# Kernel tuning notes

Measured on AMD Instinct MI355X. Metric: run time of the kernel, lower is better.

## Reference

```python
import jax, jax.numpy as jnp
import numpy as np

B, I, H, O = 65536, 128, 256, 256

def setup_inputs() -> dict:
    key = jax.random.key(0)
    ks = jax.random.split(key, 6)
    s_h = 1.0 / np.sqrt(I + H)
    return {
        "input": jax.random.normal(ks[0], (B, I), jnp.float32),
        "hidden": jax.random.normal(ks[1], (B, H), jnp.float32),
        "w_i2h": jax.random.uniform(ks[2], (4 * H, I + H), jnp.float32, -s_h, s_h),
        "b_i2h": jax.random.uniform(ks[3], (4 * H,), jnp.float32, -s_h, s_h),
        "w_i2o": jax.random.uniform(ks[4], (O, I + H), jnp.float32, -s_h, s_h),
        "b_i2o": jax.random.uniform(ks[5], (O,), jnp.float32, -s_h, s_h),
    }

def reference(input, hidden, w_i2h, b_i2h, w_i2o, b_i2o):
    # combined: [B, I+H]
    combined = jnp.concatenate([input, hidden], axis=1)
    gates = combined @ w_i2h.T + b_i2h            # [B, 4H]
    h, ig, fg, og = jnp.split(gates, 4, axis=1)   # each [B, H]
    ig = jax.nn.sigmoid(ig)
    fg = jax.nn.sigmoid(fg)
    og = jax.nn.sigmoid(og)
    h = jnp.tanh(h)
    new_hidden = og * jnp.tanh(fg * hidden + ig * h)
    output = jax.nn.log_softmax(combined @ w_i2o.T + b_i2o, axis=1)  # [B, O]
    return (output, new_hidden)
```

## Files before the change

kernel.cpp:

```cpp
#include <hip/hip_runtime.h>
#include <hip/hip_bf16.h>
#include <math.h>


typedef __attribute__((ext_vector_type(8))) short bf16x8;
typedef __attribute__((ext_vector_type(4))) float f32x4;

#define BM   64
#define NW1  393216
#define NW2  98304

__device__ __forceinline__ unsigned short f2bf(float f) {
    union { __hip_bfloat16 h; unsigned short u; } cv;
    cv.h = __float2bfloat16(f);
    return cv.u;
}
__device__ __forceinline__ float bf2f(unsigned short u) {
    union { __hip_bfloat16 h; unsigned short u; } cv;
    cv.u = u;
    return __bfloat162float(cv.h);
}
__device__ __forceinline__ float fsigmoid(float x) {
    return 1.0f / (1.0f + __expf(-x));
}
__device__ __forceinline__ float ftanh(float x) {
    return 1.0f - 2.0f / (__expf(2.0f * x) + 1.0f);
}
__device__ __forceinline__ bf16x8 pack8(float4 v0, float4 v1) {
    bf16x8 r;
    r[0] = (short)f2bf(v0.x); r[1] = (short)f2bf(v0.y);
    r[2] = (short)f2bf(v0.z); r[3] = (short)f2bf(v0.w);
    r[4] = (short)f2bf(v1.x); r[5] = (short)f2bf(v1.y);
    r[6] = (short)f2bf(v1.z); r[7] = (short)f2bf(v1.w);
    return r;
}

__global__ void conv_w(const float* __restrict__ w1, const float* __restrict__ w2,
                       unsigned short* __restrict__ wb) {
    int idx = blockIdx.x * 256 + threadIdx.x;
    const int n1 = NW1 / 4;
    float4 v;
    if (idx < n1) v = ((const float4*)w1)[idx];
    else          v = ((const float4*)w2)[idx - n1];
    ushort4 u;
    u.x = f2bf(v.x); u.y = f2bf(v.y); u.z = f2bf(v.z); u.w = f2bf(v.w);
    ((ushort4*)wb)[idx] = u;
}

__device__ __forceinline__ int lds_off(int row, int g) {
    return row * 768 + ((g ^ (row & 7)) << 4);
}

__launch_bounds__(256, 3)
__global__ void lstm_fused(const float* __restrict__ input,
                           const float* __restrict__ hidden,
                           const unsigned short* __restrict__ w1b,
                           const unsigned short* __restrict__ w2b,
                           const float* __restrict__ b1,
                           const float* __restrict__ b2,
                           float* __restrict__ out_ls,
                           float* __restrict__ out_nh)
{
    __shared__ __align__(16) unsigned short Ash[BM * 384];
    __shared__ float red_m[4][BM];
    __shared__ float red_s[4][BM];
    char* Ab = (char*)Ash;

    const int tid  = threadIdx.x;
    const int wave = tid >> 6;
    const int lane = tid & 63;
    const int l15  = lane & 15;
    const int quad = lane >> 4;
    const int rx   = l15 & 7;
    const size_t r0 = (size_t)blockIdx.x * BM;

    #pragma unroll
    for (int it = 0; it < 12; ++it) {
        int idx = it * 256 + tid;
        int row = idx / 48, g = idx % 48;
        const float* src = (g < 16) ? (input  + (r0 + row) * 128 + g * 8)
                                    : (hidden + (r0 + row) * 256 + (g - 16) * 8);
        float4 v0 = ((const float4*)src)[0];
        float4 v1 = ((const float4*)src)[1];
        *(bf16x8*)(Ab + lds_off(row, g)) = pack8(v0, v1);
    }
    __syncthreads();

    const int abase = l15 * 768;

    for (int phase = 0; phase < 5; ++phase) {
        f32x4 acc[4][4];
        #pragma unroll
        for (int i = 0; i < 4; ++i)
            #pragma unroll
            for (int j = 0; j < 4; ++j)
                acc[i][j] = (f32x4){0.f, 0.f, 0.f, 0.f};

        const unsigned short* bp[4];
        if (phase < 4) {
            int j0 = phase * 64 + wave * 16;
            #pragma unroll
            for (int q = 0; q < 4; ++q)
                bp[q] = w1b + (size_t)(q * 256 + j0 + l15) * 384 + quad * 8;
        } else {
            #pragma unroll
            for (int nt = 0; nt < 4; ++nt)
                bp[nt] = w2b + (size_t)(wave * 64 + nt * 16 + l15) * 384 + quad * 8;
        }

        auto loadB = [&](bf16x8* b, int kk) {
            #pragma unroll
            for (int nt = 0; nt < 4; ++nt)
                b[nt] = *(const bf16x8*)(bp[nt] + kk);
        };
        auto loadA = [&](bf16x8* a, int kk) {
            int go = (((kk >> 3) + quad) ^ rx) << 4;
            #pragma unroll
            for (int mt = 0; mt < 4; ++mt)
                a[mt] = *(const bf16x8*)(Ab + abase + mt * 12288 + go);
        };
        auto mfmas = [&](bf16x8* a, bf16x8* b) {
            #pragma unroll
            for (int mt = 0; mt < 4; ++mt)
                #pragma unroll
                for (int nt = 0; nt < 4; ++nt)
                    acc[mt][nt] = __builtin_amdgcn_mfma_f32_16x16x32_bf16(
                        a[mt], b[nt], acc[mt][nt], 0, 0, 0);
        };

        bf16x8 b0[4], b1f[4], a0[4], a1[4];
        loadB(b0, 0);
        #pragma unroll
        for (int kk = 0; kk < 384; kk += 64) {
            loadB(b1f, kk + 32);
            loadA(a0, kk);
            mfmas(a0, b0);
            if (kk + 64 < 384) loadB(b0, kk + 64);
            loadA(a1, kk + 32);
            mfmas(a1, b1f);
        }

        if (phase < 4) {
            int j = phase * 64 + wave * 16 + l15;
            float bq0 = b1[j], bq1 = b1[256 + j], bq2 = b1[512 + j], bq3 = b1[768 + j];
            int e = 128 + j, ge = e >> 3, oe = (e & 7) * 2;
            #pragma unroll
            for (int mt = 0; mt < 4; ++mt) {
                #pragma unroll
                for (int r = 0; r < 4; ++r) {
                    int rowl = mt * 16 + quad * 4 + r;
                    float hprev = bf2f(*(const unsigned short*)
                                       (Ab + lds_off(rowl, ge) + oe));
                    float hv  = ftanh(acc[mt][0][r] + bq0);
                    float igv = fsigmoid(acc[mt][1][r] + bq1);
                    float fgv = fsigmoid(acc[mt][2][r] + bq2);
                    float ogv = fsigmoid(acc[mt][3][r] + bq3);
                    out_nh[(r0 + rowl) * 256 + j] = ogv * ftanh(fgv * hprev + igv * hv);
                }
            }
        } else {
            float bo[4];
            #pragma unroll
            for (int nt = 0; nt < 4; ++nt) bo[nt] = b2[wave * 64 + nt * 16 + l15];
            #pragma unroll
            for (int mt = 0; mt < 4; ++mt)
                #pragma unroll
                for (int nt = 0; nt < 4; ++nt)
                    #pragma unroll
                    for (int r = 0; r < 4; ++r)
                        acc[mt][nt][r] += bo[nt];

            float pm[4][4], ps[4][4];
            #pragma unroll
            for (int mt = 0; mt < 4; ++mt)
                #pragma unroll
                for (int r = 0; r < 4; ++r) {
                    float m = acc[mt][0][r];
                    #pragma unroll
                    for (int nt = 1; nt < 4; ++nt) m = fmaxf(m, acc[mt][nt][r]);
                    pm[mt][r] = m;
                }
            #pragma unroll
            for (int mask = 1; mask < 16; mask <<= 1)
                #pragma unroll
                for (int mt = 0; mt < 4; ++mt)
                    #pragma unroll
                    for (int r = 0; r < 4; ++r)
                        pm[mt][r] = fmaxf(pm[mt][r], __shfl_xor(pm[mt][r], mask, 64));
            #pragma unroll
            for (int mt = 0; mt < 4; ++mt)
                #pragma unroll
                for (int r = 0; r < 4; ++r) {
                    float s = 0.f;
                    #pragma unroll
                    for (int nt = 0; nt < 4; ++nt)
                        s += __expf(acc[mt][nt][r] - pm[mt][r]);
                    ps[mt][r] = s;
                }
            #pragma unroll
            for (int mask = 1; mask < 16; mask <<= 1)
                #pragma unroll
                for (int mt = 0; mt < 4; ++mt)
                    #pragma unroll
                    for (int r = 0; r < 4; ++r)
                        ps[mt][r] += __shfl_xor(ps[mt][r], mask, 64);

            if (l15 == 0) {
                #pragma unroll
                for (int mt = 0; mt < 4; ++mt)
                    #pragma unroll
                    for (int r = 0; r < 4; ++r) {
                        int rowl = mt * 16 + quad * 4 + r;
                        red_m[wave][rowl] = pm[mt][r];
                        red_s[wave][rowl] = ps[mt][r];
                    }
            }
            __syncthreads();
            #pragma unroll
            for (int mt = 0; mt < 4; ++mt)
                #pragma unroll
                for (int r = 0; r < 4; ++r) {
                    int rowl = mt * 16 + quad * 4 + r;
                    float M = red_m[0][rowl];
                    #pragma unroll
                    for (int w = 1; w < 4; ++w) M = fmaxf(M, red_m[w][rowl]);
                    float S = 0.f;
                    #pragma unroll
                    for (int w = 0; w < 4; ++w)
                        S += red_s[w][rowl] * __expf(red_m[w][rowl] - M);
                    float lz = M + logf(S);
                    #pragma unroll
                    for (int nt = 0; nt < 4; ++nt)
                        out_ls[(r0 + rowl) * 256 + wave * 64 + nt * 16 + l15] =
                            acc[mt][nt][r] - lz;
                }
        }
    }
}

extern "C" void kernel_launch(void* const* d_in, const int* in_sizes, int n_in,
                              void* d_out, int out_size, void* d_ws, size_t ws_size,
                              hipStream_t stream) {
    const float* input  = (const float*)d_in[0];
    const float* hidden = (const float*)d_in[1];
    const float* w1     = (const float*)d_in[2];
    const float* b1     = (const float*)d_in[3];
    const float* w2     = (const float*)d_in[4];
    const float* b2     = (const float*)d_in[5];
    float* out = (float*)d_out;
    unsigned short* wb = (unsigned short*)d_ws;

    conv_w<<<dim3((NW1 + NW2) / 4 / 256), dim3(256), 0, stream>>>(w1, w2, wb);
    lstm_fused<<<dim3(65536 / BM), dim3(256), 0, stream>>>(
        input, hidden, wb, wb + NW1, b1, b2,
        out, out + (size_t)65536 * 256);
}
```

Before: 377.5 us.

## Split each block's rows across two wave groups with 512 threads

New measurement: 442.1 us. 1.17x slower.

```diff
diff --git a/kernel.cpp b/kernel.cpp
--- a/kernel.cpp
+++ b/kernel.cpp
@@ -51,7 +51,7 @@
     return row * 768 + ((g ^ (row & 7)) << 4);
 }
 
-__launch_bounds__(256, 3)
+__launch_bounds__(512, 4)
 __global__ void lstm_fused(const float* __restrict__ input,
                            const float* __restrict__ hidden,
                            const unsigned short* __restrict__ w1b,
@@ -68,6 +68,8 @@
 
     const int tid  = threadIdx.x;
     const int wave = tid >> 6;
+    const int wj   = wave & 3;
+    const int mh   = wave >> 2;
     const int lane = tid & 63;
     const int l15  = lane & 15;
     const int quad = lane >> 4;
@@ -75,8 +77,8 @@
     const size_t r0 = (size_t)blockIdx.x * BM;
 
     #pragma unroll
-    for (int it = 0; it < 12; ++it) {
-        int idx = it * 256 + tid;
+    for (int it = 0; it < 6; ++it) {
+        int idx = it * 512 + tid;
         int row = idx / 48, g = idx % 48;
         const float* src = (g < 16) ? (input  + (r0 + row) * 128 + g * 8)
                                     : (hidden + (r0 + row) * 256 + (g - 16) * 8);
@@ -86,26 +88,26 @@
     }
     __syncthreads();
 
-    const int abase = l15 * 768;
+    const int abase = (mh * 32 + l15) * 768;
 
     for (int phase = 0; phase < 5; ++phase) {
-        f32x4 acc[4][4];
+        f32x4 acc[2][4];
         #pragma unroll
-        for (int i = 0; i < 4; ++i)
+        for (int i = 0; i < 2; ++i)
             #pragma unroll
             for (int j = 0; j < 4; ++j)
                 acc[i][j] = (f32x4){0.f, 0.f, 0.f, 0.f};
 
         const unsigned short* bp[4];
         if (phase < 4) {
-            int j0 = phase * 64 + wave * 16;
+            int j0 = phase * 64 + wj * 16;
             #pragma unroll
             for (int q = 0; q < 4; ++q)
                 bp[q] = w1b + (size_t)(q * 256 + j0 + l15) * 384 + quad * 8;
         } else {
             #pragma unroll
             for (int nt = 0; nt < 4; ++nt)
-                bp[nt] = w2b + (size_t)(wave * 64 + nt * 16 + l15) * 384 + quad * 8;
+                bp[nt] = w2b + (size_t)(wj * 64 + nt * 16 + l15) * 384 + quad * 8;
         }
 
         auto loadB = [&](bf16x8* b, int kk) {
@@ -116,39 +118,39 @@
         auto loadA = [&](bf16x8* a, int kk) {
             int go = (((kk >> 3) + quad) ^ rx) << 4;
             #pragma unroll
-            for (int mt = 0; mt < 4; ++mt)
+            for (int mt = 0; mt < 2; ++mt)
                 a[mt] = *(const bf16x8*)(Ab + abase + mt * 12288 + go);
         };
         auto mfmas = [&](bf16x8* a, bf16x8* b) {
             #pragma unroll
-            for (int mt = 0; mt < 4; ++mt)
+            for (int mt = 0; mt < 2; ++mt)
                 #pragma unroll
                 for (int nt = 0; nt < 4; ++nt)
                     acc[mt][nt] = __builtin_amdgcn_mfma_f32_16x16x32_bf16(
                         a[mt], b[nt], acc[mt][nt], 0, 0, 0);
         };
 
-        bf16x8 b0[4], b1f[4], a0[4], a1[4];
+        bf16x8 b0[4], b1f[4], a[2];
         loadB(b0, 0);
         #pragma unroll
         for (int kk = 0; kk < 384; kk += 64) {
             loadB(b1f, kk + 32);
-            loadA(a0, kk);
-            mfmas(a0, b0);
+            loadA(a, kk);
+            mfmas(a, b0);
             if (kk + 64 < 384) loadB(b0, kk + 64);
-            loadA(a1, kk + 32);
-            mfmas(a1, b1f);
+            loadA(a, kk + 32);
+            mfmas(a, b1f);
         }
 
         if (phase < 4) {
-            int j = phase * 64 + wave * 16 + l15;
+            int j = phase * 64 + wj * 16 + l15;
             float bq0 = b1[j], bq1 = b1[256 + j], bq2 = b1[512 + j], bq3 = b1[768 + j];
             int e = 128 + j, ge = e >> 3, oe = (e & 7) * 2;
             #pragma unroll
-            for (int mt = 0; mt < 4; ++mt) {
-                #pragma unroll
-                for (int r = 0; r < 4; ++r) {
-                    int rowl = mt * 16 + quad * 4 + r;
+            for (int mt = 0; mt < 2; ++mt) {
+                #pragma unroll
+                for (int r = 0; r < 4; ++r) {
+                    int rowl = mh * 32 + mt * 16 + quad * 4 + r;
                     float hprev = bf2f(*(const unsigned short*)
                                        (Ab + lds_off(rowl, ge) + oe));
                     float hv  = ftanh(acc[mt][0][r] + bq0);
@@ -161,18 +163,18 @@
         } else {
             float bo[4];
             #pragma unroll
-            for (int nt = 0; nt < 4; ++nt) bo[nt] = b2[wave * 64 + nt * 16 + l15];
-            #pragma unroll
-            for (int mt = 0; mt < 4; ++mt)
+            for (int nt = 0; nt < 4; ++nt) bo[nt] = b2[wj * 64 + nt * 16 + l15];
+            #pragma unroll
+            for (int mt = 0; mt < 2; ++mt)
                 #pragma unroll
                 for (int nt = 0; nt < 4; ++nt)
                     #pragma unroll
                     for (int r = 0; r < 4; ++r)
                         acc[mt][nt][r] += bo[nt];
 
-            float pm[4][4], ps[4][4];
-            #pragma unroll
-            for (int mt = 0; mt < 4; ++mt)
+            float pm[2][4], ps[2][4];
+            #pragma unroll
+            for (int mt = 0; mt < 2; ++mt)
                 #pragma unroll
                 for (int r = 0; r < 4; ++r) {
                     float m = acc[mt][0][r];
@@ -183,12 +185,12 @@
             #pragma unroll
             for (int mask = 1; mask < 16; mask <<= 1)
                 #pragma unroll
-                for (int mt = 0; mt < 4; ++mt)
+                for (int mt = 0; mt < 2; ++mt)
                     #pragma unroll
                     for (int r = 0; r < 4; ++r)
                         pm[mt][r] = fmaxf(pm[mt][r], __shfl_xor(pm[mt][r], mask, 64));
             #pragma unroll
-            for (int mt = 0; mt < 4; ++mt)
+            for (int mt = 0; mt < 2; ++mt)
                 #pragma unroll
                 for (int r = 0; r < 4; ++r) {
                     float s = 0.f;
@@ -200,27 +202,27 @@
             #pragma unroll
             for (int mask = 1; mask < 16; mask <<= 1)
                 #pragma unroll
-                for (int mt = 0; mt < 4; ++mt)
+                for (int mt = 0; mt < 2; ++mt)
                     #pragma unroll
                     for (int r = 0; r < 4; ++r)
                         ps[mt][r] += __shfl_xor(ps[mt][r], mask, 64);
 
             if (l15 == 0) {
                 #pragma unroll
-                for (int mt = 0; mt < 4; ++mt)
+                for (int mt = 0; mt < 2; ++mt)
                     #pragma unroll
                     for (int r = 0; r < 4; ++r) {
-                        int rowl = mt * 16 + quad * 4 + r;
-                        red_m[wave][rowl] = pm[mt][r];
-                        red_s[wave][rowl] = ps[mt][r];
+                        int rowl = mh * 32 + mt * 16 + quad * 4 + r;
+                        red_m[wj][rowl] = pm[mt][r];
+                        red_s[wj][rowl] = ps[mt][r];
                     }
             }
             __syncthreads();
             #pragma unroll
-            for (int mt = 0; mt < 4; ++mt)
-                #pragma unroll
-                for (int r = 0; r < 4; ++r) {
-                    int rowl = mt * 16 + quad * 4 + r;
+            for (int mt = 0; mt < 2; ++mt)
+                #pragma unroll
+                for (int r = 0; r < 4; ++r) {
+                    int rowl = mh * 32 + mt * 16 + quad * 4 + r;
                     float M = red_m[0][rowl];
                     #pragma unroll
                     for (int w = 1; w < 4; ++w) M = fmaxf(M, red_m[w][rowl]);
@@ -231,7 +233,7 @@
                     float lz = M + logf(S);
                     #pragma unroll
                     for (int nt = 0; nt < 4; ++nt)
-                        out_ls[(r0 + rowl) * 256 + wave * 64 + nt * 16 + l15] =
+                        out_ls[(r0 + rowl) * 256 + wj * 64 + nt * 16 + l15] =
                             acc[mt][nt][r] - lz;
                 }
         }
@@ -251,7 +253,7 @@
     unsigned short* wb = (unsigned short*)d_ws;
 
     conv_w<<<dim3((NW1 + NW2) / 4 / 256), dim3(256), 0, stream>>>(w1, w2, wb);
-    lstm_fused<<<dim3(65536 / BM), dim3(256), 0, stream>>>(
+    lstm_fused<<<dim3(65536 / BM), dim3(512), 0, stream>>>(
         input, hidden, wb, wb + NW1, b1, b2,
         out, out + (size_t)65536 * 256);
 }
```
